# Performance work log

Measured on AMD Instinct MI355X. Metric: run time of the kernel, lower is better.

The kernel has to match this reference:

```python
import jax, jax.numpy as jnp
import numpy as np

D_MODEL = 512
H = 8
DK = D_MODEL // H  # 64


def setup_inputs() -> dict:
    key = jax.random.key(0)
    ks = jax.random.split(key, 8)
    B, S = 2, 4096
    q = jax.random.normal(ks[0], (B, S, D_MODEL), dtype=jnp.float32)
    k = jax.random.normal(ks[1], (B, S, D_MODEL), dtype=jnp.float32)
    v = jax.random.normal(ks[2], (B, S, D_MODEL), dtype=jnp.float32)
    # per-head projection weights, torch nn.Linear layout [out, in], stacked over heads
    scale = 1.0 / np.sqrt(D_MODEL)
    Wq = jax.random.uniform(ks[3], (H, DK, D_MODEL), jnp.float32, -scale, scale)
    Wk = jax.random.uniform(ks[4], (H, DK, D_MODEL), jnp.float32, -scale, scale)
    Wv = jax.random.uniform(ks[5], (H, DK, D_MODEL), jnp.float32, -scale, scale)
    Wo = jax.random.uniform(ks[6], (D_MODEL, D_MODEL), jnp.float32, -scale, scale)
    # causal mask (True = keep), matches masked_fill(mask.logical_not(), -inf)
    mask = jnp.tril(jnp.ones((S, S), dtype=jnp.bool_))
    return {"q": q, "k": k, "v": v, "Wq": Wq, "Wk": Wk, "Wv": Wv, "Wo": Wo, "mask": mask}


def reference(q, k, v, Wq, Wk, Wv, Wo, mask):
    # per-head projections (stacked): x @ W^T for each head -> [B, H, S, DK]
    qh = jnp.einsum('bsd,hed->bhse', q, Wq)
    kh = jnp.einsum('bsd,hed->bhse', k, Wk)
    vh = jnp.einsum('bsd,hed->bhse', v, Wv)
    scaling = 1.0 / np.sqrt(DK)
    scores = jnp.einsum('bhse,bhte->bhst', qh, kh) * scaling  # [B,H,S,S]
    scores = jnp.where(mask, scores, -jnp.inf)
    attn = jax.nn.softmax(scores, axis=-1)
    heads = jnp.einsum('bhst,bhte->bhse', attn, vh)  # [B,H,S,DK]
    B, _, S, _ = heads.shape
    concat = jnp.transpose(heads, (0, 2, 1, 3)).reshape(B, S, D_MODEL)
    return concat @ Wo.T
```

## Files before the change

### kernel.cpp

```cpp
#include <hip/hip_runtime.h>
#include <hip/hip_bf16.h>
#include <math.h>

typedef __bf16 bf16_t;
typedef __bf16 bf16x8 __attribute__((ext_vector_type(8)));
typedef __bf16 bf16x4 __attribute__((ext_vector_type(4)));
typedef short short4v __attribute__((ext_vector_type(4)));
typedef float f32x4 __attribute__((ext_vector_type(4)));

__device__ __forceinline__ f32x4 mfma_k32(bf16x8 a, bf16x8 b, f32x4 c) {
    return __builtin_amdgcn_mfma_f32_16x16x32_bf16(a, b, c, 0, 0, 0);
}

__device__ __forceinline__ f32x4 mfma_k16(bf16x4 a, bf16x4 b, f32x4 c) {
#if __has_builtin(__builtin_amdgcn_mfma_f32_16x16x16_bf16)
    return __builtin_amdgcn_mfma_f32_16x16x16_bf16(a, b, c, 0, 0, 0);
#elif __has_builtin(__builtin_amdgcn_mfma_f32_16x16x16bf16_1k)
    short4v as, bs;
    __builtin_memcpy(&as, &a, 8);
    __builtin_memcpy(&bs, &b, 8);
    return __builtin_amdgcn_mfma_f32_16x16x16bf16_1k(as, bs, c, 0, 0, 0);
#else
    f32x4 d = c;
    asm volatile("v_mfma_f32_16x16x16_bf16 %0, %1, %2, %0" : "+v"(d) : "v"(a), "v"(b));
    return d;
#endif
}

__device__ __forceinline__ float fast_exp2(float x) {
#if __has_builtin(__builtin_amdgcn_exp2f)
    return __builtin_amdgcn_exp2f(x);
#else
    float r;
    asm("v_exp_f32 %0, %1" : "=v"(r) : "v"(x));
    return r;
#endif
}

__device__ __forceinline__ void async16(const bf16_t* g, __bf16* l) {
    __builtin_amdgcn_global_load_lds(
        (const __attribute__((address_space(1))) void*)g,
        (__attribute__((address_space(3))) void*)l, 16, 0, 0);
}

__device__ __forceinline__ int swz_col(int col, int row) {
    return (col & ~63) | ((((col >> 3) & 7) ^ (row & 7)) << 3) | (col & 7);
}

__device__ __forceinline__ bf16x8 cvt8(float4 a, float4 b) {
    bf16x8 w;
    w[0]=(__bf16)a.x; w[1]=(__bf16)a.y; w[2]=(__bf16)a.z; w[3]=(__bf16)a.w;
    w[4]=(__bf16)b.x; w[5]=(__bf16)b.y; w[6]=(__bf16)b.z; w[7]=(__bf16)b.w;
    return w;
}

__global__ __launch_bounds__(256) void cvt_W(const float* __restrict__ Wq,
                                             const float* __restrict__ Wk,
                                             const float* __restrict__ Wv,
                                             const float* __restrict__ Wo,
                                             bf16_t* __restrict__ Wc) {
    const int b2 = blockIdx.x;
    const int m = b2 >> 7;
    const float* src = m == 0 ? Wq : m == 1 ? Wk : m == 2 ? Wv : Wo;
    const float sc = (m == 0) ? 0.125f * 1.44269504088896f : 1.0f;
    size_t i = ((size_t)(b2 & 127) * 256 + threadIdx.x) * 8;
    int row = (int)(i >> 9), col = (int)(i & 511);
    float4 a0 = *(const float4*)(src + i), a1 = *(const float4*)(src + i + 4);
    bf16x8 o;
    o[0]=(__bf16)(a0.x*sc); o[1]=(__bf16)(a0.y*sc); o[2]=(__bf16)(a0.z*sc); o[3]=(__bf16)(a0.w*sc);
    o[4]=(__bf16)(a1.x*sc); o[5]=(__bf16)(a1.y*sc); o[6]=(__bf16)(a1.z*sc); o[7]=(__bf16)(a1.w*sc);
    *(bf16x8*)(Wc + (size_t)m * 262144 + (size_t)row * 512 + swz_col(col, row)) = o;
}

template<int MODE, int AF32, int BF32>
__device__ __forceinline__ void gemm128_body(const bf16_t* __restrict__ Ab,
                                             const float* __restrict__ Af,
                                             const bf16_t* __restrict__ Bb,
                                             const float* __restrict__ Bf,
                                             void* __restrict__ outp,
                                             int m0, int n0) {
    __shared__ __bf16 Asm[128 * 64];
    __shared__ __bf16 Bsm[128 * 64];
    const int tid  = threadIdx.x;
    const int wave = tid >> 6;
    const int lane = tid & 63;
    const int quad = lane >> 4;
    const int l16  = lane & 15;
    const int swz  = l16 & 7;
    const int r8 = lane >> 3;
    const int c8 = (lane & 7) * 8;
    const int mrow0 = (wave & 1) * 64;
    const int ncol0 = (wave >> 1) * 64;

    f32x4 acc[4][4];
    for (int i = 0; i < 4; ++i)
        for (int j = 0; j < 4; ++j) acc[i][j] = (f32x4){0.f, 0.f, 0.f, 0.f};

    for (int kt = 0; kt < 512; kt += 64) {
        __syncthreads();
        for (int j = 0; j < 4; ++j) {
            const int rl = wave * 32 + j * 8 + r8;
            if (AF32) {
                const float* s = Af + (size_t)(m0 + rl) * 512 + kt + c8;
                float4 v0 = *(const float4*)s, v1 = *(const float4*)(s + 4);
                *(bf16x8*)&Asm[rl * 64 + (((lane & 7) ^ r8) << 3)] = cvt8(v0, v1);
            } else {
                async16(Ab + (size_t)(m0 + rl) * 512 + kt + c8,
                        &Asm[(wave * 32 + j * 8) * 64]);
            }
            if (BF32) {
                const float* s = Bf + (size_t)(n0 + rl) * 512 + kt + c8;
                float4 v0 = *(const float4*)s, v1 = *(const float4*)(s + 4);
                *(bf16x8*)&Bsm[rl * 64 + (((lane & 7) ^ r8) << 3)] = cvt8(v0, v1);
            } else {
                async16(Bb + (size_t)(n0 + rl) * 512 + kt + c8,
                        &Bsm[(wave * 32 + j * 8) * 64]);
            }
        }
        __syncthreads();

        for (int ks = 0; ks < 2; ++ks) {
            bf16x8 af[4];
            for (int mt = 0; mt < 4; ++mt)
                af[mt] = *(const bf16x8*)&Asm[(mrow0 + mt * 16 + l16) * 64 + ((ks * 4 + quad) ^ swz) * 8];
            for (int nt = 0; nt < 4; ++nt) {
                bf16x8 bf = *(const bf16x8*)&Bsm[(ncol0 + nt * 16 + l16) * 64 + ((ks * 4 + quad) ^ swz) * 8];
                for (int mt = 0; mt < 4; ++mt)
                    acc[mt][nt] = mfma_k32(af[mt], bf, acc[mt][nt]);
            }
        }
    }

    if (MODE == 0) {
        bf16_t* out = (bf16_t*)outp;
        for (int nt = 0; nt < 4; ++nt) {
            int e = n0 + ncol0 + nt * 16 + l16;
            int h = e >> 6, el = e & 63;
            for (int mt = 0; mt < 4; ++mt)
                for (int r = 0; r < 4; ++r) {
                    int row = m0 + mrow0 + mt * 16 + quad * 4 + r;
                    int b = row >> 12, s = row & 4095;
                    int elp = (((el >> 3) ^ (row & 7)) << 3) | (el & 7);
                    out[(((size_t)(b * 8 + h)) * 4096 + s) * 64 + elp] = (bf16_t)acc[mt][nt][r];
                }
        }
    } else {
        bf16_t* out = (bf16_t*)outp;
        for (int nt = 0; nt < 4; ++nt) {
            int s_g = n0 + ncol0 + nt * 16 + l16;
            int b = s_g >> 12;
            int sbase = (s_g & 4095) & ~63;
            int f = 16 * ((l16 >> 2) & 3) + 4 * nt + (l16 & 3);
            for (int mt = 0; mt < 4; ++mt)
                for (int r = 0; r < 4; ++r) {
                    int e_g = m0 + mrow0 + mt * 16 + quad * 4 + r;
                    int h = e_g >> 6, el = e_g & 63;
                    int col = sbase | ((((f >> 3) ^ (e_g & 7)) & 7) << 3) | (f & 7);
                    out[(((size_t)(b * 8 + h)) * 64 + el) * 4096 + col] = (bf16_t)acc[mt][nt][r];
                }
        }
    }
}

__global__ __launch_bounds__(256) void proj_fused(const float* __restrict__ q,
                                                  const float* __restrict__ k,
                                                  const float* __restrict__ v,
                                                  const bf16_t* __restrict__ Wc,
                                                  bf16_t* __restrict__ qh,
                                                  bf16_t* __restrict__ kh,
                                                  bf16_t* __restrict__ vh) {
    const int f = blockIdx.x;
    const int y = (f >> 3) & 3;
    const int x = (f & 7) | ((f >> 5) << 3);
    const int z = blockIdx.z;
    const bf16_t* W = Wc + (size_t)z * 262144;
    if (z == 0)
        gemm128_body<0, 1, 0>(nullptr, q, W, nullptr, qh, x * 128, y * 128);
    else if (z == 1)
        gemm128_body<0, 1, 0>(nullptr, k, W, nullptr, kh, x * 128, y * 128);
    else
        gemm128_body<1, 0, 1>(W, nullptr, nullptr, v, vh, y * 128, x * 128);
}

__global__ __launch_bounds__(256) void gemm_final(const bf16_t* __restrict__ Op,
                                                  const float* __restrict__ Lp,
                                                  const bf16_t* __restrict__ B,
                                                  float* __restrict__ out) {
    __shared__ __bf16 Asm[128 * 64];
    __shared__ __bf16 Bsm[128 * 64];
    const int fb = blockIdx.x;
    const int m0 = ((fb & 7) | ((fb >> 5) << 3)) * 128;
    const int n0 = ((fb >> 3) & 3) * 128;
    const int tid  = threadIdx.x;
    const int wave = tid >> 6;
    const int lane = tid & 63;
    const int quad = lane >> 4;
    const int l16  = lane & 15;
    const int swz  = l16 & 7;
    const int r8 = lane >> 3;
    const int c8 = (lane & 7) * 8;
    const int mrow0 = (wave & 1) * 64;
    const int ncol0 = (wave >> 1) * 64;

    f32x4 acc[4][4];
    for (int i = 0; i < 4; ++i)
        for (int j = 0; j < 4; ++j) acc[i][j] = (f32x4){0.f, 0.f, 0.f, 0.f};

    for (int kt = 0; kt < 512; kt += 64) {
        const int h = kt >> 6;
        __syncthreads();
        for (int j = 0; j < 4; ++j)
            async16(B + (size_t)(n0 + wave * 32 + j * 8 + r8) * 512 + kt + c8,
                    &Bsm[(wave * 32 + j * 8) * 64]);
        for (int j = 0; j < 4; ++j) {
            const int rl  = wave * 32 + j * 8 + r8;
            const int row = m0 + rl;
            const int b   = row >> 12, sp = row & 4095;
            const size_t lidx = (size_t)(b * 8 + h) * 4096 + sp;
            bf16x8 a0 = *(const bf16x8*)(Op + lidx * 64 + c8);
            bf16x8 a1 = *(const bf16x8*)(Op + 4194304 + lidx * 64 + c8);
            float inv = 1.0f / (Lp[lidx] + Lp[65536 + lidx]);
            bf16x8 w;
            for (int i = 0; i < 8; ++i)
                w[i] = (bf16_t)(((float)a0[i] + (float)a1[i]) * inv);
            *(bf16x8*)&Asm[rl * 64 + (((lane & 7) ^ r8) << 3)] = w;
        }
        __syncthreads();

        for (int ks = 0; ks < 2; ++ks) {
            bf16x8 af[4];
            for (int mt = 0; mt < 4; ++mt)
                af[mt] = *(const bf16x8*)&Asm[(mrow0 + mt * 16 + l16) * 64 + ((ks * 4 + quad) ^ swz) * 8];
            for (int nt = 0; nt < 4; ++nt) {
                bf16x8 bf = *(const bf16x8*)&Bsm[(ncol0 + nt * 16 + l16) * 64 + ((ks * 4 + quad) ^ swz) * 8];
                for (int mt = 0; mt < 4; ++mt)
                    acc[mt][nt] = mfma_k32(af[mt], bf, acc[mt][nt]);
            }
        }
    }

    for (int nt = 0; nt < 4; ++nt) {
        int n = n0 + ncol0 + nt * 16 + l16;
        for (int mt = 0; mt < 4; ++mt)
            for (int r = 0; r < 4; ++r) {
                int row = m0 + mrow0 + mt * 16 + quad * 4 + r;
                out[(size_t)row * 512 + n] = acc[mt][nt][r];
            }
    }
}

__global__ __launch_bounds__(256, 4) void attn_kernel(const bf16_t* __restrict__ qh,
                                                      const bf16_t* __restrict__ kh,
                                                      const bf16_t* __restrict__ vh,
                                                      bf16_t* __restrict__ Opart,
                                                      float* __restrict__ Lpart) {
    __shared__ __bf16 SM[16384];
    __bf16* KSM = &SM[0];
    __bf16* VSM = &SM[8192];
    float* Osc = (float*)SM;
    float* Lsc = (float*)&SM[8320];

    const int id   = blockIdx.x;
    const int bh   = ((id & 7) << 1) | ((id >> 3) & 1);
    const int pair = (id >> 4) & 31;
    const int z    = (id >> 9) & 1;

    const int tid  = threadIdx.x;
    const int wave = tid >> 6;
    const int g2   = wave >> 1;
    const int wl   = wave & 1;
    const int lane = tid & 63;
    const int quad = lane >> 4;
    const int l16  = lane & 15;
    const int swz  = l16 & 7;
    const size_t base = (size_t)bh * 4096 * 64;
    const int r8 = lane >> 3;
    const int c8 = (lane & 7) * 8;

    bf16_t* Op = Opart + (size_t)z * 4194304;
    float*  Lp = Lpart + z * 65536;

    for (int leg = 0; leg < 2; ++leg) {
        const int qt = leg ? (63 - pair) : pair;
        const int q0 = qt * 64;

        bf16x8 qf[2][2];
        for (int g = 0; g < 2; ++g) {
            const bf16_t* qp = qh + base + (size_t)(q0 + wl * 32 + g * 16 + l16) * 64;
            qf[g][0] = *(const bf16x8*)(qp + ((quad ^ swz) * 8));
            qf[g][1] = *(const bf16x8*)(qp + (((4 + quad) ^ swz) * 8));
        }

        f32x4 o[2][4];
        for (int g = 0; g < 2; ++g)
            for (int i = 0; i < 4; ++i) o[g][i] = (f32x4){0.f, 0.f, 0.f, 0.f};
        float lsum[2] = {0.f, 0.f};

        const int S  = (qt + 2) >> 1;
        const int Sh = (S + 1) >> 1;
        const int it0 = z ? Sh : 0;
        const int it1 = z ? S : Sh;

        for (int it = it0; it < it1; ++it) {
            const int j0 = it * 128;
            __syncthreads();
            for (int p = 0; p < 2; ++p)
                for (int j = 0; j < 2; ++j) {
                    int row = wave * 16 + j * 8 + r8;
                    async16(kh + base + (size_t)(j0 + p * 64 + row) * 64 + c8,
                            KSM + (p * 64 + wave * 16 + j * 8) * 64);
                    async16(vh + (size_t)(bh * 64 + row) * 4096 + j0 + p * 64 + c8,
                            VSM + (p * 64 + wave * 16 + j * 8) * 64);
                }
            __syncthreads();

            const int pp = g2;
            const int koff = j0 + pp * 64 - q0;
            if (koff > wl * 32 + 31) continue;

            f32x4 st[2][4];
            for (int nt = 0; nt < 4; ++nt) {
                const __bf16* kr = KSM + (pp * 64 + nt * 16 + l16) * 64;
                bf16x8 kf0 = *(const bf16x8*)(kr + ((quad ^ swz) * 8));
                bf16x8 kf1 = *(const bf16x8*)(kr + (((4 + quad) ^ swz) * 8));
                for (int g = 0; g < 2; ++g) {
                    f32x4 zz = (f32x4){0.f, 0.f, 0.f, 0.f};
                    zz = mfma_k32(kf0, qf[g][0], zz);
                    zz = mfma_k32(kf1, qf[g][1], zz);
                    st[g][nt] = zz;
                }
            }

            bf16x4 pf[2][4];
            for (int g = 0; g < 2; ++g) {
                const int qb = wl * 32 + g * 16;
                if (koff + 63 <= qb) {
                    for (int nt = 0; nt < 4; ++nt)
                        for (int r = 0; r < 4; ++r) {
                            float p = fast_exp2(st[g][nt][r]);
                            lsum[g] += p;
                            pf[g][nt][r] = (bf16_t)p;
                        }
                } else {
                    const int qrow = qb + l16;
                    for (int nt = 0; nt < 4; ++nt)
                        for (int r = 0; r < 4; ++r) {
                            int key = nt * 16 + quad * 4 + r;
                            float p = (key + koff <= qrow) ? fast_exp2(st[g][nt][r]) : 0.f;
                            lsum[g] += p;
                            pf[g][nt][r] = (bf16_t)p;
                        }
                }
            }

            for (int dt = 0; dt < 4; ++dt)
                for (int kt2 = 0; kt2 < 2; ++kt2) {
                    bf16x8 vf = *(const bf16x8*)&VSM[(pp * 64 + dt * 16 + l16) * 64 + (((2 * quad + kt2) ^ swz) * 8)];
                    bf16x4 vlo = {vf[0], vf[1], vf[2], vf[3]};
                    bf16x4 vhi = {vf[4], vf[5], vf[6], vf[7]};
                    for (int g = 0; g < 2; ++g) {
                        o[g][dt] = mfma_k16(pf[g][2 * kt2], vlo, o[g][dt]);
                        o[g][dt] = mfma_k16(pf[g][2 * kt2 + 1], vhi, o[g][dt]);
                    }
                }
        }

        __syncthreads();
        if (g2 == 1) {
            for (int g = 0; g < 2; ++g) {
                float ls = lsum[g];
                ls += __shfl_xor(ls, 16);
                ls += __shfl_xor(ls, 32);
                const int qb = wl * 32 + g * 16;
                Lsc[qb + l16] = ls;
                for (int dt = 0; dt < 4; ++dt)
                    for (int r = 0; r < 4; ++r)
                        Osc[(qb + quad * 4 + r) * 65 + dt * 16 + l16] = o[g][dt][r];
            }
        }
        __syncthreads();
        if (g2 == 0) {
            for (int g = 0; g < 2; ++g) {
                float ls = lsum[g];
                ls += __shfl_xor(ls, 16);
                ls += __shfl_xor(ls, 32);
                const int qb = wl * 32 + g * 16;
                ls += Lsc[qb + l16];
                Lsc[qb + l16] = ls;
                for (int dt = 0; dt < 4; ++dt)
                    for (int r = 0; r < 4; ++r) {
                        int idx = (qb + quad * 4 + r) * 65 + dt * 16 + l16;
                        Osc[idx] = o[g][dt][r] + Osc[idx];
                    }
            }
        }
        __syncthreads();
        {
            const int q  = tid >> 2;
            const int e0 = (tid & 3) * 16;
            bf16x8 w0, w1;
            for (int i = 0; i < 8; ++i) {
                w0[i] = (bf16_t)Osc[q * 65 + e0 + i];
                w1[i] = (bf16_t)Osc[q * 65 + e0 + 8 + i];
            }
            size_t slot = ((size_t)(bh * 64 + qt)) * 4096 + q * 64 + e0;
            *(bf16x8*)&Op[slot]     = w0;
            *(bf16x8*)&Op[slot + 8] = w1;
            if (tid < 64) Lp[(bh * 64 + qt) * 64 + tid] = Lsc[tid];
        }
    }
}

extern "C" void kernel_launch(void* const* d_in, const int* in_sizes, int n_in,
                              void* d_out, int out_size, void* d_ws, size_t ws_size,
                              hipStream_t stream) {
    const float* q  = (const float*)d_in[0];
    const float* k  = (const float*)d_in[1];
    const float* v  = (const float*)d_in[2];
    const float* Wq = (const float*)d_in[3];
    const float* Wk = (const float*)d_in[4];
    const float* Wv = (const float*)d_in[5];
    const float* Wo = (const float*)d_in[6];
    float* out = (float*)d_out;

    bf16_t* ws = (bf16_t*)d_ws;
    const size_t R = (size_t)8192 * 512;
    bf16_t* opart = ws + R;
    bf16_t* vh = ws + 3 * R;
    bf16_t* Wc = ws + 4 * R;
    float*  Lp = (float*)(ws + 4 * R + 1048576);
    bf16_t* qh = (bf16_t*)d_out;
    bf16_t* kh = (bf16_t*)d_out + R;

    cvt_W<<<dim3(512), dim3(256), 0, stream>>>(Wq, Wk, Wv, Wo, Wc);
    proj_fused<<<dim3(256, 1, 3), dim3(256), 0, stream>>>(q, k, v, Wc, qh, kh, vh);
    attn_kernel<<<dim3(1024), dim3(256), 0, stream>>>(qh, kh, vh, opart, Lp);
    gemm_final<<<dim3(256), dim3(256), 0, stream>>>(opart, Lp, Wc + 3 * 262144, out);
}
```

Measured before the change: 239.2 us.

## Double-buffer LDS tiles in projection and output GEMMs with register prefetch

Converts the projection GEMM and the final output GEMM to double-buffered shared memory. The next K-tile's global loads (fp32 into registers, or async copies for bf16) are issued before the MFMA loop on the current buffer, and the converted data is written to LDS at the start of the next iteration. This removes one barrier per iteration and overlaps global memory latency with compute. In exchange it doubles LDS use to 64KB per block and raises register pressure, with launch bounds set to 2 blocks per CU.

```diff
diff --git a/kernel.cpp b/kernel.cpp
--- a/kernel.cpp
+++ b/kernel.cpp
@@ -73,14 +73,14 @@
 }
 
 template<int MODE, int AF32, int BF32>
-__device__ __forceinline__ void gemm128_body(const bf16_t* __restrict__ Ab,
+__device__ __forceinline__ void gemm128_dbuf(const bf16_t* __restrict__ Ab,
                                              const float* __restrict__ Af,
                                              const bf16_t* __restrict__ Bb,
                                              const float* __restrict__ Bf,
                                              void* __restrict__ outp,
                                              int m0, int n0) {
-    __shared__ __bf16 Asm[128 * 64];
-    __shared__ __bf16 Bsm[128 * 64];
+    __shared__ __bf16 Asm[2][128 * 64];
+    __shared__ __bf16 Bsm[2][128 * 64];
     const int tid  = threadIdx.x;
     const int wave = tid >> 6;
     const int lane = tid & 63;
@@ -91,40 +91,75 @@
     const int c8 = (lane & 7) * 8;
     const int mrow0 = (wave & 1) * 64;
     const int ncol0 = (wave >> 1) * 64;
+    const int wswz = ((lane & 7) ^ r8) << 3;
 
     f32x4 acc[4][4];
     for (int i = 0; i < 4; ++i)
         for (int j = 0; j < 4; ++j) acc[i][j] = (f32x4){0.f, 0.f, 0.f, 0.f};
 
-    for (int kt = 0; kt < 512; kt += 64) {
+    float4 apre[4][2], bpre[4][2];
+
+#pragma unroll
+    for (int j = 0; j < 4; ++j) {
+        const int rl = wave * 32 + j * 8 + r8;
+        if (AF32) {
+            const float* s = Af + (size_t)(m0 + rl) * 512 + c8;
+            apre[j][0] = *(const float4*)s; apre[j][1] = *(const float4*)(s + 4);
+        } else {
+            async16(Ab + (size_t)(m0 + rl) * 512 + c8, &Asm[0][(wave * 32 + j * 8) * 64]);
+        }
+        if (BF32) {
+            const float* s = Bf + (size_t)(n0 + rl) * 512 + c8;
+            bpre[j][0] = *(const float4*)s; bpre[j][1] = *(const float4*)(s + 4);
+        } else {
+            async16(Bb + (size_t)(n0 + rl) * 512 + c8, &Bsm[0][(wave * 32 + j * 8) * 64]);
+        }
+    }
+
+    for (int it = 0; it < 8; ++it) {
+        const int cb = it & 1;
+        if (AF32) {
+#pragma unroll
+            for (int j = 0; j < 4; ++j) {
+                const int rl = wave * 32 + j * 8 + r8;
+                *(bf16x8*)&Asm[cb][rl * 64 + wswz] = cvt8(apre[j][0], apre[j][1]);
+            }
+        }
+        if (BF32) {
+#pragma unroll
+            for (int j = 0; j < 4; ++j) {
+                const int rl = wave * 32 + j * 8 + r8;
+                *(bf16x8*)&Bsm[cb][rl * 64 + wswz] = cvt8(bpre[j][0], bpre[j][1]);
+            }
+        }
         __syncthreads();
-        for (int j = 0; j < 4; ++j) {
-            const int rl = wave * 32 + j * 8 + r8;
-            if (AF32) {
-                const float* s = Af + (size_t)(m0 + rl) * 512 + kt + c8;
-                float4 v0 = *(const float4*)s, v1 = *(const float4*)(s + 4);
-                *(bf16x8*)&Asm[rl * 64 + (((lane & 7) ^ r8) << 3)] = cvt8(v0, v1);
-            } else {
-                async16(Ab + (size_t)(m0 + rl) * 512 + kt + c8,
-                        &Asm[(wave * 32 + j * 8) * 64]);
-            }
-            if (BF32) {
-                const float* s = Bf + (size_t)(n0 + rl) * 512 + kt + c8;
-                float4 v0 = *(const float4*)s, v1 = *(const float4*)(s + 4);
-                *(bf16x8*)&Bsm[rl * 64 + (((lane & 7) ^ r8) << 3)] = cvt8(v0, v1);
-            } else {
-                async16(Bb + (size_t)(n0 + rl) * 512 + kt + c8,
-                        &Bsm[(wave * 32 + j * 8) * 64]);
-            }
-        }
-        __syncthreads();
-
+        if (it < 7) {
+            const int ktn = (it + 1) * 64;
+#pragma unroll
+            for (int j = 0; j < 4; ++j) {
+                const int rl = wave * 32 + j * 8 + r8;
+                if (AF32) {
+                    const float* s = Af + (size_t)(m0 + rl) * 512 + ktn + c8;
+                    apre[j][0] = *(const float4*)s; apre[j][1] = *(const float4*)(s + 4);
+                } else {
+                    async16(Ab + (size_t)(m0 + rl) * 512 + ktn + c8,
+                            &Asm[cb ^ 1][(wave * 32 + j * 8) * 64]);
+                }
+                if (BF32) {
+                    const float* s = Bf + (size_t)(n0 + rl) * 512 + ktn + c8;
+                    bpre[j][0] = *(const float4*)s; bpre[j][1] = *(const float4*)(s + 4);
+                } else {
+                    async16(Bb + (size_t)(n0 + rl) * 512 + ktn + c8,
+                            &Bsm[cb ^ 1][(wave * 32 + j * 8) * 64]);
+                }
+            }
+        }
         for (int ks = 0; ks < 2; ++ks) {
             bf16x8 af[4];
             for (int mt = 0; mt < 4; ++mt)
-                af[mt] = *(const bf16x8*)&Asm[(mrow0 + mt * 16 + l16) * 64 + ((ks * 4 + quad) ^ swz) * 8];
+                af[mt] = *(const bf16x8*)&Asm[cb][(mrow0 + mt * 16 + l16) * 64 + ((ks * 4 + quad) ^ swz) * 8];
             for (int nt = 0; nt < 4; ++nt) {
-                bf16x8 bf = *(const bf16x8*)&Bsm[(ncol0 + nt * 16 + l16) * 64 + ((ks * 4 + quad) ^ swz) * 8];
+                bf16x8 bf = *(const bf16x8*)&Bsm[cb][(ncol0 + nt * 16 + l16) * 64 + ((ks * 4 + quad) ^ swz) * 8];
                 for (int mt = 0; mt < 4; ++mt)
                     acc[mt][nt] = mfma_k32(af[mt], bf, acc[mt][nt]);
             }
@@ -162,32 +197,32 @@
     }
 }
 
-__global__ __launch_bounds__(256) void proj_fused(const float* __restrict__ q,
-                                                  const float* __restrict__ k,
-                                                  const float* __restrict__ v,
-                                                  const bf16_t* __restrict__ Wc,
-                                                  bf16_t* __restrict__ qh,
-                                                  bf16_t* __restrict__ kh,
-                                                  bf16_t* __restrict__ vh) {
+__global__ __launch_bounds__(256, 2) void proj_fused(const float* __restrict__ q,
+                                                     const float* __restrict__ k,
+                                                     const float* __restrict__ v,
+                                                     const bf16_t* __restrict__ Wc,
+                                                     bf16_t* __restrict__ qh,
+                                                     bf16_t* __restrict__ kh,
+                                                     bf16_t* __restrict__ vh) {
     const int f = blockIdx.x;
     const int y = (f >> 3) & 3;
     const int x = (f & 7) | ((f >> 5) << 3);
     const int z = blockIdx.z;
     const bf16_t* W = Wc + (size_t)z * 262144;
     if (z == 0)
-        gemm128_body<0, 1, 0>(nullptr, q, W, nullptr, qh, x * 128, y * 128);
+        gemm128_dbuf<0, 1, 0>(nullptr, q, W, nullptr, qh, x * 128, y * 128);
     else if (z == 1)
-        gemm128_body<0, 1, 0>(nullptr, k, W, nullptr, kh, x * 128, y * 128);
+        gemm128_dbuf<0, 1, 0>(nullptr, k, W, nullptr, kh, x * 128, y * 128);
     else
-        gemm128_body<1, 0, 1>(W, nullptr, nullptr, v, vh, y * 128, x * 128);
-}
-
-__global__ __launch_bounds__(256) void gemm_final(const bf16_t* __restrict__ Op,
-                                                  const float* __restrict__ Lp,
-                                                  const bf16_t* __restrict__ B,
-                                                  float* __restrict__ out) {
-    __shared__ __bf16 Asm[128 * 64];
-    __shared__ __bf16 Bsm[128 * 64];
+        gemm128_dbuf<1, 0, 1>(W, nullptr, nullptr, v, vh, y * 128, x * 128);
+}
+
+__global__ __launch_bounds__(256, 2) void gemm_final(const bf16_t* __restrict__ Op,
+                                                     const float* __restrict__ Lp,
+                                                     const bf16_t* __restrict__ B,
+                                                     float* __restrict__ out) {
+    __shared__ __bf16 Asm[2][128 * 64];
+    __shared__ __bf16 Bsm[2][128 * 64];
     const int fb = blockIdx.x;
     const int m0 = ((fb & 7) | ((fb >> 5) << 3)) * 128;
     const int n0 = ((fb >> 3) & 3) * 128;
@@ -201,38 +236,60 @@
     const int c8 = (lane & 7) * 8;
     const int mrow0 = (wave & 1) * 64;
     const int ncol0 = (wave >> 1) * 64;
+    const int wswz = ((lane & 7) ^ r8) << 3;
 
     f32x4 acc[4][4];
     for (int i = 0; i < 4; ++i)
         for (int j = 0; j < 4; ++j) acc[i][j] = (f32x4){0.f, 0.f, 0.f, 0.f};
 
-    for (int kt = 0; kt < 512; kt += 64) {
-        const int h = kt >> 6;
-        __syncthreads();
-        for (int j = 0; j < 4; ++j)
-            async16(B + (size_t)(n0 + wave * 32 + j * 8 + r8) * 512 + kt + c8,
-                    &Bsm[(wave * 32 + j * 8) * 64]);
+    bf16x8 oa0[4], oa1[4];
+    float oinv[4];
+
+#pragma unroll
+    for (int j = 0; j < 4; ++j) {
+        const int rl = wave * 32 + j * 8 + r8;
+        const int row = m0 + rl;
+        const int b = row >> 12, sp = row & 4095;
+        const size_t lidx = (size_t)(b * 8) * 4096 + sp;
+        oa0[j] = *(const bf16x8*)(Op + lidx * 64 + c8);
+        oa1[j] = *(const bf16x8*)(Op + 4194304 + lidx * 64 + c8);
+        oinv[j] = 1.0f / (Lp[lidx] + Lp[65536 + lidx]);
+        async16(B + (size_t)(n0 + rl) * 512 + c8, &Bsm[0][(wave * 32 + j * 8) * 64]);
+    }
+
+    for (int it = 0; it < 8; ++it) {
+        const int cb = it & 1;
+#pragma unroll
         for (int j = 0; j < 4; ++j) {
-            const int rl  = wave * 32 + j * 8 + r8;
-            const int row = m0 + rl;
-            const int b   = row >> 12, sp = row & 4095;
-            const size_t lidx = (size_t)(b * 8 + h) * 4096 + sp;
-            bf16x8 a0 = *(const bf16x8*)(Op + lidx * 64 + c8);
-            bf16x8 a1 = *(const bf16x8*)(Op + 4194304 + lidx * 64 + c8);
-            float inv = 1.0f / (Lp[lidx] + Lp[65536 + lidx]);
+            const int rl = wave * 32 + j * 8 + r8;
             bf16x8 w;
             for (int i = 0; i < 8; ++i)
-                w[i] = (bf16_t)(((float)a0[i] + (float)a1[i]) * inv);
-            *(bf16x8*)&Asm[rl * 64 + (((lane & 7) ^ r8) << 3)] = w;
+                w[i] = (bf16_t)(((float)oa0[j][i] + (float)oa1[j][i]) * oinv[j]);
+            *(bf16x8*)&Asm[cb][rl * 64 + wswz] = w;
         }
         __syncthreads();
-
+        if (it < 7) {
+            const int hn = it + 1;
+            const int ktn = hn * 64;
+#pragma unroll
+            for (int j = 0; j < 4; ++j) {
+                const int rl = wave * 32 + j * 8 + r8;
+                const int row = m0 + rl;
+                const int b = row >> 12, sp = row & 4095;
+                const size_t lidx = (size_t)(b * 8 + hn) * 4096 + sp;
+                oa0[j] = *(const bf16x8*)(Op + lidx * 64 + c8);
+                oa1[j] = *(const bf16x8*)(Op + 4194304 + lidx * 64 + c8);
+                oinv[j] = 1.0f / (Lp[lidx] + Lp[65536 + lidx]);
+                async16(B + (size_t)(n0 + rl) * 512 + ktn + c8,
+                        &Bsm[cb ^ 1][(wave * 32 + j * 8) * 64]);
+            }
+        }
         for (int ks = 0; ks < 2; ++ks) {
             bf16x8 af[4];
             for (int mt = 0; mt < 4; ++mt)
-                af[mt] = *(const bf16x8*)&Asm[(mrow0 + mt * 16 + l16) * 64 + ((ks * 4 + quad) ^ swz) * 8];
+                af[mt] = *(const bf16x8*)&Asm[cb][(mrow0 + mt * 16 + l16) * 64 + ((ks * 4 + quad) ^ swz) * 8];
             for (int nt = 0; nt < 4; ++nt) {
-                bf16x8 bf = *(const bf16x8*)&Bsm[(ncol0 + nt * 16 + l16) * 64 + ((ks * 4 + quad) ^ swz) * 8];
+                bf16x8 bf = *(const bf16x8*)&Bsm[cb][(ncol0 + nt * 16 + l16) * 64 + ((ks * 4 + quad) ^ swz) * 8];
                 for (int mt = 0; mt < 4; ++mt)
                     acc[mt][nt] = mfma_k32(af[mt], bf, acc[mt][nt]);
             }
```

Result: slower. 245.4 us (+2.6%).
